# Optimization experiments

Measured on AMD Instinct MI355X. Metric: run time of the kernel, lower is better.

## Reference

```python
import jax, jax.numpy as jnp
import numpy as np

HIDDEN = 2048
EXPERTS = 8
INTER = 1024
TOP_K = 2
AUX_LOSS_WEIGHT = 0.01
TOKENS = 8192


def setup_inputs() -> dict:
    key = jax.random.key(0)
    k_x, k_g, k_w1, k_w2 = jax.random.split(key, 4)
    x = jax.random.normal(k_x, (TOKENS, HIDDEN), dtype=jnp.float32)
    # nn.Linear(hidden, experts, bias=False): weight is [E, H], applied as x @ W^T
    gate_w = jax.random.normal(k_g, (EXPERTS, HIDDEN), dtype=jnp.float32) * 0.02
    w1 = jax.random.normal(k_w1, (EXPERTS, HIDDEN, INTER), dtype=jnp.float32) * 0.02
    w2 = jax.random.normal(k_w2, (EXPERTS, INTER, HIDDEN), dtype=jnp.float32) * 0.02
    return {"x": x, "gate_w": gate_w, "w1": w1, "w2": w2}


def _moe_forward(x, gate_w, w1, w2):
    E = gate_w.shape[0]
    logits = x @ gate_w.T                              # [T, E]
    probs = jax.nn.softmax(logits, axis=-1)            # [T, E]
    topk_w, topk_idx = jax.lax.top_k(probs, TOP_K)     # [T, K]
    topk_w = topk_w / jnp.sum(topk_w, axis=-1, keepdims=True)

    # load-balancing aux loss: E * sum_e f_e * P_e
    one_hot = jax.nn.one_hot(topk_idx, E, dtype=probs.dtype)   # [T, K, E]
    f = jnp.mean(jnp.sum(one_hot, axis=1), axis=0)             # fraction of tokens per expert
    P = jnp.mean(probs, axis=0)                                # mean router prob per expert
    aux_loss = AUX_LOSS_WEIGHT * E * jnp.sum(f * P)

    # grouped expert MLP (dense-over-experts formulation, same math as
    # permute -> grouped GEMM -> unpermute):
    h = jnp.einsum('th,ehi->tei', x, w1)               # [T, E, I]
    h = jax.nn.gelu(h)
    y = jnp.einsum('tei,eih->teh', h, w2)              # [T, E, H]

    # combine: gather each token's top-k expert outputs and weight them
    y_sel = jnp.take_along_axis(y, topk_idx[:, :, None], axis=1)  # [T, K, H]
    out = jnp.sum(y_sel * topk_w[:, :, None], axis=1)             # [T, H]
    return out, aux_loss


def reference(x, gate_w, w1, w2):
    return _moe_forward(x, gate_w, w1, w2)
```

## Files before the change

### kernel.cpp

```cpp
#include <hip/hip_runtime.h>
#include <hip/hip_fp16.h>
#include <cmath>

#define T_TOKENS 8192
#define HID 2048
#define NEXP 8
#define INTERM 1024
#define GATE_NB 2048
#define MAX_TT 136
#define GEMM1_GRID (8 * 136)
#define GEMM2_GRID (8 * 272)

typedef _Float16 f16x8 __attribute__((ext_vector_type(8)));
typedef _Float16 f16x4 __attribute__((ext_vector_type(4)));
typedef float f32x4 __attribute__((ext_vector_type(4)));

static __device__ __forceinline__ float gelu_tanh(float v) {
    return 0.5f * v * (1.0f + tanhf(0.79788456080286535588f * (v + 0.044715f * v * v * v)));
}

static __device__ __forceinline__ void glds16(const void* g, void* l) {
    __builtin_amdgcn_global_load_lds((const __attribute__((address_space(1))) void*)g,
                                     (__attribute__((address_space(3))) void*)l, 16, 0, 0);
}

static __device__ __forceinline__ f16x8 lds_read32(const _Float16* base, int row, int chunk) {
    int phys = chunk ^ ((row >> 1) & 3);
    return *reinterpret_cast<const f16x8*>(
        reinterpret_cast<const char*>(base) + row * 64 + phys * 16);
}

static __device__ __forceinline__ void tconv_body(const float* __restrict__ in,
                                                  _Float16* __restrict__ out,
                                                  int R, int C, int bx, int by, int bz) {
    __shared__ float t[32][33];
    int r0 = by * 32, c0 = bx * 32;
    int tid = threadIdx.x;
    int r = tid >> 3, c4 = (tid & 7) * 4;
    const float4 v = *reinterpret_cast<const float4*>(&in[((size_t)bz * R + (r0 + r)) * C + c0 + c4]);
    t[r][c4 + 0] = v.x; t[r][c4 + 1] = v.y; t[r][c4 + 2] = v.z; t[r][c4 + 3] = v.w;
    __syncthreads();
    int oc = tid >> 3;
    int or4 = (tid & 7) * 4;
    f16x4 o;
    o[0] = (_Float16)t[or4 + 0][oc];
    o[1] = (_Float16)t[or4 + 1][oc];
    o[2] = (_Float16)t[or4 + 2][oc];
    o[3] = (_Float16)t[or4 + 3][oc];
    *reinterpret_cast<f16x4*>(&out[((size_t)bz * C + (c0 + oc)) * R + r0 + or4]) = o;
}

static __device__ __forceinline__ void gate_body(const float* __restrict__ x,
                                                 const float* __restrict__ gw,
                                                 _Float16* __restrict__ xh,
                                                 int* __restrict__ tk_idx, float* __restrict__ tk_w,
                                                 int* __restrict__ part_cnt,
                                                 double* __restrict__ part_sumP, int gid) {
    __shared__ double sds[4][NEXP];
    __shared__ int sci[4][NEXP];
    int w = threadIdx.x >> 6;
    int lane = threadIdx.x & 63;
    int t = gid * 4 + w;

    const float4* xr = (const float4*)(x + (size_t)t * HID);
    _Float16* xo = xh + (size_t)t * HID;
    double acc[NEXP];
#pragma unroll
    for (int e = 0; e < NEXP; e++) acc[e] = 0.0;
#pragma unroll
    for (int i = 0; i < HID / 256; i++) {
        float4 xv = xr[i * 64 + lane];
        f16x4 h;
        h[0] = (_Float16)xv.x; h[1] = (_Float16)xv.y;
        h[2] = (_Float16)xv.z; h[3] = (_Float16)xv.w;
        *reinterpret_cast<f16x4*>(xo + i * 256 + lane * 4) = h;
#pragma unroll
        for (int e = 0; e < NEXP; e++) {
            float4 gv = ((const float4*)(gw + (size_t)e * HID))[i * 64 + lane];
            acc[e] += (double)xv.x * (double)gv.x + (double)xv.y * (double)gv.y
                    + (double)xv.z * (double)gv.z + (double)xv.w * (double)gv.w;
        }
    }
#pragma unroll
    for (int e = 0; e < NEXP; e++) {
#pragma unroll
        for (int off = 32; off > 0; off >>= 1) acc[e] += __shfl_xor(acc[e], off, 64);
    }
    double mx = acc[0];
#pragma unroll
    for (int e = 1; e < NEXP; e++) mx = acc[e] > mx ? acc[e] : mx;
    double ex[NEXP];
    double sum = 0.0;
#pragma unroll
    for (int e = 0; e < NEXP; e++) { ex[e] = exp(acc[e] - mx); sum += ex[e]; }
    int i0 = 0;
#pragma unroll
    for (int e = 1; e < NEXP; e++) if (ex[e] > ex[i0]) i0 = e;
    int i1 = (i0 == 0) ? 1 : 0;
#pragma unroll
    for (int e = 0; e < NEXP; e++) if (e != i0 && ex[e] > ex[i1]) i1 = e;
    double p0 = ex[i0], p1 = ex[i1];
    double t2 = p0 + p1;
    if (lane == 0) {
        tk_idx[2 * t] = i0; tk_idx[2 * t + 1] = i1;
        tk_w[2 * t] = (float)(p0 / t2); tk_w[2 * t + 1] = (float)(p1 / t2);
#pragma unroll
        for (int e = 0; e < NEXP; e++) {
            sds[w][e] = ex[e] / sum;
            sci[w][e] = (e == i0 ? 1 : 0) + (e == i1 ? 1 : 0);
        }
    }
    __syncthreads();
    if (threadIdx.x < NEXP) {
        int e = threadIdx.x;
        part_sumP[e * GATE_NB + gid] = sds[0][e] + sds[1][e] + sds[2][e] + sds[3][e];
        part_cnt[e * GATE_NB + gid]  = sci[0][e] + sci[1][e] + sci[2][e] + sci[3][e];
    }
}

__global__ __launch_bounds__(256) void prep_kernel(const float* __restrict__ x,
                                                   const float* __restrict__ gw,
                                                   const float* __restrict__ w1,
                                                   const float* __restrict__ w2,
                                                   _Float16* __restrict__ xh,
                                                   _Float16* __restrict__ w1t,
                                                   _Float16* __restrict__ w2t,
                                                   int* __restrict__ tk_idx, float* __restrict__ tk_w,
                                                   int* __restrict__ part_cnt,
                                                   double* __restrict__ part_sumP) {
    int bid = blockIdx.x;
    if (bid < 16384) {
        int bx = bid & 31, by = (bid >> 5) & 63, bz = bid >> 11;
        tconv_body(w1, w1t, HID, INTERM, bx, by, bz);
    } else if (bid < 32768) {
        int r = bid - 16384;
        int bx = r & 63, by = (r >> 6) & 31, bz = r >> 11;
        tconv_body(w2, w2t, INTERM, HID, bx, by, bz);
    } else {
        gate_body(x, gw, xh, tk_idx, tk_w, part_cnt, part_sumP, bid - 32768);
    }
}

__global__ __launch_bounds__(256) void finalize_kernel(const int* __restrict__ part_cnt,
                                                       const double* __restrict__ part_sumP,
                                                       int* __restrict__ cnt, int* __restrict__ offs,
                                                       int* __restrict__ cursor,
                                                       int* __restrict__ ttab,
                                                       int* __restrict__ nmt,
                                                       float* __restrict__ aux_out) {
    __shared__ double swv[4];
    __shared__ int cwv[4];
    __shared__ double sE[NEXP];
    __shared__ int cE[NEXP];
    int w = threadIdx.x >> 6;
    int lane = threadIdx.x & 63;
    for (int e = 0; e < NEXP; e++) {
        double s = 0.0; int c = 0;
        for (int j = threadIdx.x; j < GATE_NB; j += 256) {
            s += part_sumP[e * GATE_NB + j];
            c += part_cnt[e * GATE_NB + j];
        }
#pragma unroll
        for (int off = 32; off > 0; off >>= 1) {
            s += __shfl_xor(s, off, 64);
            c += __shfl_xor(c, off, 64);
        }
        if (lane == 0) { swv[w] = s; cwv[w] = c; }
        __syncthreads();
        if (threadIdx.x == 0) {
            sE[e] = swv[0] + swv[1] + swv[2] + swv[3];
            cE[e] = cwv[0] + cwv[1] + cwv[2] + cwv[3];
        }
        __syncthreads();
    }
    if (threadIdx.x == 0) {
        int off = 0;
        double aux = 0.0;
        int idx = 0;
#pragma unroll
        for (int e = 0; e < NEXP; e++) {
            cnt[e] = cE[e];
            offs[e] = off;
            off += cE[e];
            cursor[e] = 0;
            aux += ((double)cE[e] / (double)T_TOKENS) * (sE[e] / (double)T_TOKENS);
            int mt = (cE[e] + 127) >> 7;
            for (int m = 0; m < mt; m++) ttab[idx++] = (e << 16) | m;
        }
        nmt[0] = idx;
        for (; idx < MAX_TT; idx++) ttab[idx] = -1;
        aux_out[0] = (float)(0.01 * (double)NEXP * aux);
    }
}

__global__ void scatter_kernel(const int* __restrict__ tk_idx, const float* __restrict__ tk_w,
                               const int* __restrict__ offs, int* __restrict__ cursor,
                               int* __restrict__ row_tok, float* __restrict__ row_w,
                               int* __restrict__ tok_row) {
    int t = blockIdx.x * blockDim.x + threadIdx.x;
    int lane = threadIdx.x & 63;
    unsigned long long below = (lane == 0) ? 0ull : ((~0ull) >> (64 - lane));
    for (int k = 0; k < 2; k++) {
        int e = tk_idx[2 * t + k];
        float wv = tk_w[2 * t + k];
        int pos = 0;
#pragma unroll
        for (int ee = 0; ee < NEXP; ee++) {
            unsigned long long m = __ballot(e == ee);
            if (e == ee) {
                int rank = (int)__popcll(m & below);
                int leader = (int)__ffsll((unsigned long long)m) - 1;
                int b = 0;
                if (lane == leader) b = atomicAdd(&cursor[ee], (int)__popcll(m));
                b = __shfl(b, leader, 64);
                pos = b + rank;
            }
        }
        int r = offs[e] + pos;
        row_tok[r] = t;
        row_w[r] = wv;
        tok_row[2 * t + k] = r;
    }
}

template<bool GATHER, bool GELU, int KTOT, int NX>
__global__ __launch_bounds__(256, 4) void gemmf_kernel(
    const _Float16* __restrict__ Aglob,
    const _Float16* __restrict__ Bglob,
    const int* __restrict__ cnt, const int* __restrict__ offs,
    const int* __restrict__ row_tok,
    const int* __restrict__ ttab,
    const int* __restrict__ nmt,
    _Float16* __restrict__ Out, int Ncols)
{
    constexpr int NT = KTOT / 32;
    __shared__ __align__(16) _Float16 As[2][128][32];
    __shared__ __align__(16) _Float16 Bs[2][128][32];

    int n_items = nmt[0] * NX;
    int chunk = (n_items + 7) >> 3;
    int xcd = blockIdx.x & 7;
    int i = blockIdx.x >> 3;
    if (i >= chunk) return;
    int it = xcd * chunk + i;
    if (it >= n_items) return;

    int tid = threadIdx.x;
    int w = tid >> 6, lane = tid & 63;
    int wr = w >> 1, wc = w & 1;
    int fr = lane & 15, fq = lane >> 4;

    int srow = lane >> 2;
    int lc = (lane & 3) ^ ((lane >> 3) & 3);

    _Float16* ldsA = &As[0][0][0] + w * 1024;
    _Float16* ldsB = &Bs[0][0][0] + w * 1024;

    int ent = ttab[it / NX];
    int e = ent >> 16;
    int m0 = (ent & 0xffff) << 7;
    int Ne = cnt[e];
    int base = offs[e];
    int n0 = (it & (NX - 1)) << 7;

    const _Float16* aS[2];
#pragma unroll
    for (int g = 0; g < 2; g++) {
        int ar = m0 + w * 32 + g * 16 + srow; if (ar >= Ne) ar = Ne - 1;
        int id = GATHER ? row_tok[base + ar] : (base + ar);
        aS[g] = Aglob + (size_t)id * KTOT + lc * 8;
    }
    const size_t bexp = (size_t)e * Ncols * KTOT;
    const _Float16* bS[2];
#pragma unroll
    for (int g = 0; g < 2; g++)
        bS[g] = Bglob + bexp + (size_t)(n0 + w * 32 + g * 16 + srow) * KTOT + lc * 8;

#define STAGE1(S, KOFF) do {                                        \
        glds16(aS[0] + (KOFF), ldsA + (S) * 4096 + 0 * 512);        \
        glds16(aS[1] + (KOFF), ldsA + (S) * 4096 + 1 * 512);        \
        glds16(bS[0] + (KOFF), ldsB + (S) * 4096 + 0 * 512);        \
        glds16(bS[1] + (KOFF), ldsB + (S) * 4096 + 1 * 512);        \
    } while (0)

    f32x4 acc[4][4] = {};
    STAGE1(0, 0);

    for (int j = 0; j < NT; ++j) {
        int slot = j & 1;
        const _Float16* Ab = &As[slot][0][0];
        const _Float16* Bb = &Bs[slot][0][0];
        if (j + 1 < NT) {
            STAGE1(slot ^ 1, (j + 1) * 32);
            asm volatile("s_waitcnt vmcnt(4)" ::: "memory");
        } else {
            asm volatile("s_waitcnt vmcnt(0)" ::: "memory");
        }
        __builtin_amdgcn_s_barrier();

        f16x8 a_[4], b_[4];
#pragma unroll
        for (int ii = 0; ii < 4; ii++)
            a_[ii] = lds_read32(Ab, wr * 64 + ii * 16 + fr, fq);
#pragma unroll
        for (int jj = 0; jj < 4; jj++)
            b_[jj] = lds_read32(Bb, wc * 64 + jj * 16 + fr, fq);
#pragma unroll
        for (int ii = 0; ii < 4; ii++)
#pragma unroll
            for (int jj = 0; jj < 4; jj++)
                acc[ii][jj] = __builtin_amdgcn_mfma_f32_16x16x32_f16(
                    a_[ii], b_[jj], acc[ii][jj], 0, 0, 0);
        asm volatile("s_waitcnt lgkmcnt(0)" ::: "memory");
        __builtin_amdgcn_s_barrier();
    }
#undef STAGE1

#pragma unroll
    for (int mi = 0; mi < 4; mi++) {
#pragma unroll
        for (int r = 0; r < 4; r++) {
            int row = m0 + wr * 64 + mi * 16 + fq * 4 + r;
            if (row < Ne) {
                _Float16* dst = Out + (size_t)(base + row) * Ncols + n0 + wc * 64 + fr;
#pragma unroll
                for (int ni = 0; ni < 4; ni++) {
                    float v = acc[mi][ni][r];
                    if (GELU) v = gelu_tanh(v);
                    dst[ni * 16] = (_Float16)v;
                }
            }
        }
    }
}

__global__ __launch_bounds__(256) void combine_kernel(const _Float16* __restrict__ y,
                                                      const int* __restrict__ tok_row,
                                                      const float* __restrict__ tk_w,
                                                      float* __restrict__ out) {
    int t = blockIdx.x;
    int c = threadIdx.x;
    int r0 = tok_row[2 * t], r1 = tok_row[2 * t + 1];
    float w0 = tk_w[2 * t], w1 = tk_w[2 * t + 1];
    f16x8 a = reinterpret_cast<const f16x8*>(y + (size_t)r0 * HID)[c];
    f16x8 b = reinterpret_cast<const f16x8*>(y + (size_t)r1 * HID)[c];
    float4 o0, o1;
    o0.x = w0 * (float)a[0] + w1 * (float)b[0];
    o0.y = w0 * (float)a[1] + w1 * (float)b[1];
    o0.z = w0 * (float)a[2] + w1 * (float)b[2];
    o0.w = w0 * (float)a[3] + w1 * (float)b[3];
    o1.x = w0 * (float)a[4] + w1 * (float)b[4];
    o1.y = w0 * (float)a[5] + w1 * (float)b[5];
    o1.z = w0 * (float)a[6] + w1 * (float)b[6];
    o1.w = w0 * (float)a[7] + w1 * (float)b[7];
    float4* dst = reinterpret_cast<float4*>(out + (size_t)t * HID + c * 8);
    dst[0] = o0;
    dst[1] = o1;
}

extern "C" void kernel_launch(void* const* d_in, const int* in_sizes, int n_in,
                              void* d_out, int out_size, void* d_ws, size_t ws_size,
                              hipStream_t stream) {
    const float* x  = (const float*)d_in[0];
    const float* gw = (const float*)d_in[1];
    const float* w1 = (const float*)d_in[2];
    const float* w2 = (const float*)d_in[3];
    float* out = (float*)d_out;
    char* ws = (char*)d_ws;

    int*    cnt       = (int*)(ws + 0);
    int*    cursor    = (int*)(ws + 64);
    int*    offs      = (int*)(ws + 128);
    int*    nmt       = (int*)(ws + 256);
    int*    ttab      = (int*)(ws + 512);
    int*    part_cnt  = (int*)(ws + 4096);
    double* part_sumP = (double*)(ws + 131072);
    int*    row_tok   = (int*)(ws + 262144);
    float*  row_w     = (float*)(ws + 327680);
    int*    tk_idx    = (int*)(ws + 393216);
    float*  tk_w      = (float*)(ws + 458752);
    int*    tok_row   = (int*)(ws + 524288);
    const size_t OFF = 589824;
    _Float16* xh  = (_Float16*)(ws + OFF);
    _Float16* w1t = (_Float16*)(ws + OFF + (1ull << 25));
    _Float16* w2t = (_Float16*)(ws + OFF + (2ull << 25));
    _Float16* hh  = (_Float16*)(ws + OFF + (3ull << 25));
    _Float16* y   = (_Float16*)(ws + OFF);

    prep_kernel<<<32768 + GATE_NB, 256, 0, stream>>>(x, gw, w1, w2, xh, w1t, w2t,
                                                     tk_idx, tk_w, part_cnt, part_sumP);
    finalize_kernel<<<1, 256, 0, stream>>>(part_cnt, part_sumP, cnt, offs, cursor,
                                           ttab, nmt, out + (size_t)T_TOKENS * HID);
    scatter_kernel<<<T_TOKENS / 256, 256, 0, stream>>>(tk_idx, tk_w, offs, cursor,
                                                       row_tok, row_w, tok_row);

    gemmf_kernel<true, true, HID, INTERM / 128>
        <<<GEMM1_GRID, 256, 0, stream>>>(xh, w1t, cnt, offs, row_tok, ttab, nmt, hh, INTERM);
    gemmf_kernel<false, false, INTERM, HID / 128>
        <<<GEMM2_GRID, 256, 0, stream>>>(hh, w2t, cnt, offs, row_tok, ttab, nmt, y, HID);

    combine_kernel<<<T_TOKENS, 256, 0, stream>>>(y, tok_row, tk_w, out);
}
```

Before: 378.2 us.

## Overlap w2 transpose with first expert GEMM and use single-buffered GEMM2

After: 372.9 us. No clear change (-1.4%).

```diff
diff --git a/kernel.cpp b/kernel.cpp
--- a/kernel.cpp
+++ b/kernel.cpp
@@ -9,6 +9,7 @@
 #define GATE_NB 2048
 #define MAX_TT 136
 #define GEMM1_GRID (8 * 136)
+#define W2_BLOCKS 16384
 #define GEMM2_GRID (8 * 272)
 
 typedef _Float16 f16x8 __attribute__((ext_vector_type(8)));
@@ -32,21 +33,22 @@
 
 static __device__ __forceinline__ void tconv_body(const float* __restrict__ in,
                                                   _Float16* __restrict__ out,
-                                                  int R, int C, int bx, int by, int bz) {
-    __shared__ float t[32][33];
+                                                  int R, int C, int bx, int by, int bz,
+                                                  float* __restrict__ t ) {
     int r0 = by * 32, c0 = bx * 32;
     int tid = threadIdx.x;
     int r = tid >> 3, c4 = (tid & 7) * 4;
     const float4 v = *reinterpret_cast<const float4*>(&in[((size_t)bz * R + (r0 + r)) * C + c0 + c4]);
-    t[r][c4 + 0] = v.x; t[r][c4 + 1] = v.y; t[r][c4 + 2] = v.z; t[r][c4 + 3] = v.w;
+    t[r * 33 + c4 + 0] = v.x; t[r * 33 + c4 + 1] = v.y;
+    t[r * 33 + c4 + 2] = v.z; t[r * 33 + c4 + 3] = v.w;
     __syncthreads();
     int oc = tid >> 3;
     int or4 = (tid & 7) * 4;
     f16x4 o;
-    o[0] = (_Float16)t[or4 + 0][oc];
-    o[1] = (_Float16)t[or4 + 1][oc];
-    o[2] = (_Float16)t[or4 + 2][oc];
-    o[3] = (_Float16)t[or4 + 3][oc];
+    o[0] = (_Float16)t[(or4 + 0) * 33 + oc];
+    o[1] = (_Float16)t[(or4 + 1) * 33 + oc];
+    o[2] = (_Float16)t[(or4 + 2) * 33 + oc];
+    o[3] = (_Float16)t[(or4 + 3) * 33 + oc];
     *reinterpret_cast<f16x4*>(&out[((size_t)bz * C + (c0 + oc)) * R + r0 + or4]) = o;
 }
 
@@ -121,23 +123,18 @@
 __global__ __launch_bounds__(256) void prep_kernel(const float* __restrict__ x,
                                                    const float* __restrict__ gw,
                                                    const float* __restrict__ w1,
-                                                   const float* __restrict__ w2,
                                                    _Float16* __restrict__ xh,
                                                    _Float16* __restrict__ w1t,
-                                                   _Float16* __restrict__ w2t,
                                                    int* __restrict__ tk_idx, float* __restrict__ tk_w,
                                                    int* __restrict__ part_cnt,
                                                    double* __restrict__ part_sumP) {
+    __shared__ float tsh[32 * 33];
     int bid = blockIdx.x;
     if (bid < 16384) {
         int bx = bid & 31, by = (bid >> 5) & 63, bz = bid >> 11;
-        tconv_body(w1, w1t, HID, INTERM, bx, by, bz);
-    } else if (bid < 32768) {
-        int r = bid - 16384;
-        int bx = r & 63, by = (r >> 6) & 31, bz = r >> 11;
-        tconv_body(w2, w2t, INTERM, HID, bx, by, bz);
+        tconv_body(w1, w1t, HID, INTERM, bx, by, bz, tsh);
     } else {
-        gate_body(x, gw, xh, tk_idx, tk_w, part_cnt, part_sumP, bid - 32768);
+        gate_body(x, gw, xh, tk_idx, tk_w, part_cnt, part_sumP, bid - 16384);
     }
 }
 
@@ -223,7 +220,7 @@
     }
 }
 
-template<bool GATHER, bool GELU, int KTOT, int NX>
+template<bool GATHER, bool GELU, int KTOT, int NX, bool FUSE>
 __global__ __launch_bounds__(256, 4) void gemmf_kernel(
     const _Float16* __restrict__ Aglob,
     const _Float16* __restrict__ Bglob,
@@ -231,11 +228,20 @@
     const int* __restrict__ row_tok,
     const int* __restrict__ ttab,
     const int* __restrict__ nmt,
-    _Float16* __restrict__ Out, int Ncols)
+    _Float16* __restrict__ Out, int Ncols,
+    const float* __restrict__ w2in, _Float16* __restrict__ w2out)
 {
     constexpr int NT = KTOT / 32;
     __shared__ __align__(16) _Float16 As[2][128][32];
     __shared__ __align__(16) _Float16 Bs[2][128][32];
+
+    if (FUSE && blockIdx.x >= GEMM1_GRID) {
+        int b = blockIdx.x - GEMM1_GRID;
+        int bx = b & 63, by = (b >> 6) & 31, bz = b >> 11;
+        tconv_body(w2in, w2out, INTERM, HID, bx, by, bz,
+                   reinterpret_cast<float*>(&As[0][0][0]));
+        return;
+    }
 
     int n_items = nmt[0] * NX;
     int chunk = (n_items + 7) >> 3;
@@ -329,6 +335,98 @@
                     if (GELU) v = gelu_tanh(v);
                     dst[ni * 16] = (_Float16)v;
                 }
+            }
+        }
+    }
+}
+
+template<int KTOT, int NX>
+__global__ __launch_bounds__(256, 4) void gemms_kernel(
+    const _Float16* __restrict__ Aglob,
+    const _Float16* __restrict__ Bglob,
+    const int* __restrict__ cnt, const int* __restrict__ offs,
+    const int* __restrict__ ttab,
+    const int* __restrict__ nmt,
+    _Float16* __restrict__ Out, int Ncols)
+{
+    constexpr int NT = KTOT / 32;
+    __shared__ __align__(16) _Float16 As[128][32];
+    __shared__ __align__(16) _Float16 Bs[128][32];
+
+    int n_items = nmt[0] * NX;
+    int chunk = (n_items + 7) >> 3;
+    int xcd = blockIdx.x & 7;
+    int i = blockIdx.x >> 3;
+    if (i >= chunk) return;
+    int it = xcd * chunk + i;
+    if (it >= n_items) return;
+
+    int tid = threadIdx.x;
+    int w = tid >> 6, lane = tid & 63;
+    int wr = w >> 1, wc = w & 1;
+    int fr = lane & 15, fq = lane >> 4;
+
+    int srow = lane >> 2;
+    int lc = (lane & 3) ^ ((lane >> 3) & 3);
+
+    _Float16* ldsA = &As[0][0] + w * 1024;
+    _Float16* ldsB = &Bs[0][0] + w * 1024;
+
+    int ent = ttab[it / NX];
+    int e = ent >> 16;
+    int m0 = (ent & 0xffff) << 7;
+    int Ne = cnt[e];
+    int base = offs[e];
+    int n0 = (it & (NX - 1)) << 7;
+
+    const _Float16* aS[2];
+#pragma unroll
+    for (int g = 0; g < 2; g++) {
+        int ar = m0 + w * 32 + g * 16 + srow; if (ar >= Ne) ar = Ne - 1;
+        aS[g] = Aglob + (size_t)(base + ar) * KTOT + lc * 8;
+    }
+    const size_t bexp = (size_t)e * Ncols * KTOT;
+    const _Float16* bS[2];
+#pragma unroll
+    for (int g = 0; g < 2; g++)
+        bS[g] = Bglob + bexp + (size_t)(n0 + w * 32 + g * 16 + srow) * KTOT + lc * 8;
+
+    f32x4 acc[4][4] = {};
+
+    for (int j = 0; j < NT; ++j) {
+        int koff = j * 32;
+        glds16(aS[0] + koff, ldsA + 0 * 512);
+        glds16(aS[1] + koff, ldsA + 1 * 512);
+        glds16(bS[0] + koff, ldsB + 0 * 512);
+        glds16(bS[1] + koff, ldsB + 1 * 512);
+        __syncthreads();
+
+        f16x8 a_[4], b_[4];
+#pragma unroll
+        for (int ii = 0; ii < 4; ii++)
+            a_[ii] = lds_read32(&As[0][0], wr * 64 + ii * 16 + fr, fq);
+#pragma unroll
+        for (int jj = 0; jj < 4; jj++)
+            b_[jj] = lds_read32(&Bs[0][0], wc * 64 + jj * 16 + fr, fq);
+#pragma unroll
+        for (int ii = 0; ii < 4; ii++)
+#pragma unroll
+            for (int jj = 0; jj < 4; jj++)
+                acc[ii][jj] = __builtin_amdgcn_mfma_f32_16x16x32_f16(
+                    a_[ii], b_[jj], acc[ii][jj], 0, 0, 0);
+        __syncthreads();
+    }
+
+#pragma unroll
+    for (int mi = 0; mi < 4; mi++) {
+#pragma unroll
+        for (int r = 0; r < 4; r++) {
+            int row = m0 + wr * 64 + mi * 16 + fq * 4 + r;
+            if (row < Ne) {
+                _Float16* dst = Out + (size_t)(base + row) * Ncols + n0 + wc * 64 + fr;
+#pragma unroll
+                for (int ni = 0; ni < 4; ni++)
+                    dst[ni * 16] = (_Float16)acc[mi][ni][r];
             }
         }
     }
@@ -387,17 +485,18 @@
     _Float16* hh  = (_Float16*)(ws + OFF + (3ull << 25));
     _Float16* y   = (_Float16*)(ws + OFF);
 
-    prep_kernel<<<32768 + GATE_NB, 256, 0, stream>>>(x, gw, w1, w2, xh, w1t, w2t,
+    prep_kernel<<<16384 + GATE_NB, 256, 0, stream>>>(x, gw, w1, xh, w1t,
                                                      tk_idx, tk_w, part_cnt, part_sumP);
     finalize_kernel<<<1, 256, 0, stream>>>(part_cnt, part_sumP, cnt, offs, cursor,
                                            ttab, nmt, out + (size_t)T_TOKENS * HID);
     scatter_kernel<<<T_TOKENS / 256, 256, 0, stream>>>(tk_idx, tk_w, offs, cursor,
                                                        row_tok, row_w, tok_row);
 
-    gemmf_kernel<true, true, HID, INTERM / 128>
-        <<<GEMM1_GRID, 256, 0, stream>>>(xh, w1t, cnt, offs, row_tok, ttab, nmt, hh, INTERM);
-    gemmf_kernel<false, false, INTERM, HID / 128>
-        <<<GEMM2_GRID, 256, 0, stream>>>(hh, w2t, cnt, offs, row_tok, ttab, nmt, y, HID);
+    gemmf_kernel<true, true, HID, INTERM / 128, true>
+        <<<GEMM1_GRID + W2_BLOCKS, 256, 0, stream>>>(xh, w1t, cnt, offs, row_tok, ttab, nmt,
+                                                     hh, INTERM, w2, w2t);
+    gemms_kernel<INTERM, HID / 128>
+        <<<GEMM2_GRID, 256, 0, stream>>>(hh, w2t, cnt, offs, ttab, nmt, y, HID);
 
     combine_kernel<<<T_TOKENS, 256, 0, stream>>>(y, tok_row, tk_w, out);
 }
```

## Overlap w2 transpose with first expert GEMM and use single-buffered BK=64 tiles

Applied to the files above, without the earlier changes.

Result: faster. 333.7 us (-11.8%).

```diff
diff --git a/kernel.cpp b/kernel.cpp
--- a/kernel.cpp
+++ b/kernel.cpp
@@ -9,6 +9,7 @@
 #define GATE_NB 2048
 #define MAX_TT 136
 #define GEMM1_GRID (8 * 136)
+#define W2_BLOCKS 16384
 #define GEMM2_GRID (8 * 272)
 
 typedef _Float16 f16x8 __attribute__((ext_vector_type(8)));
@@ -24,29 +25,30 @@
                                      (__attribute__((address_space(3))) void*)l, 16, 0, 0);
 }
 
-static __device__ __forceinline__ f16x8 lds_read32(const _Float16* base, int row, int chunk) {
-    int phys = chunk ^ ((row >> 1) & 3);
+static __device__ __forceinline__ f16x8 lds_read(const _Float16* base, int row, int chunk) {
+    int phys = chunk ^ (row & 7);
     return *reinterpret_cast<const f16x8*>(
-        reinterpret_cast<const char*>(base) + row * 64 + phys * 16);
+        reinterpret_cast<const char*>(base) + row * 128 + phys * 16);
 }
 
 static __device__ __forceinline__ void tconv_body(const float* __restrict__ in,
                                                   _Float16* __restrict__ out,
-                                                  int R, int C, int bx, int by, int bz) {
-    __shared__ float t[32][33];
+                                                  int R, int C, int bx, int by, int bz,
+                                                  float* __restrict__ t ) {
     int r0 = by * 32, c0 = bx * 32;
     int tid = threadIdx.x;
     int r = tid >> 3, c4 = (tid & 7) * 4;
     const float4 v = *reinterpret_cast<const float4*>(&in[((size_t)bz * R + (r0 + r)) * C + c0 + c4]);
-    t[r][c4 + 0] = v.x; t[r][c4 + 1] = v.y; t[r][c4 + 2] = v.z; t[r][c4 + 3] = v.w;
+    t[r * 33 + c4 + 0] = v.x; t[r * 33 + c4 + 1] = v.y;
+    t[r * 33 + c4 + 2] = v.z; t[r * 33 + c4 + 3] = v.w;
     __syncthreads();
     int oc = tid >> 3;
     int or4 = (tid & 7) * 4;
     f16x4 o;
-    o[0] = (_Float16)t[or4 + 0][oc];
-    o[1] = (_Float16)t[or4 + 1][oc];
-    o[2] = (_Float16)t[or4 + 2][oc];
-    o[3] = (_Float16)t[or4 + 3][oc];
+    o[0] = (_Float16)t[(or4 + 0) * 33 + oc];
+    o[1] = (_Float16)t[(or4 + 1) * 33 + oc];
+    o[2] = (_Float16)t[(or4 + 2) * 33 + oc];
+    o[3] = (_Float16)t[(or4 + 3) * 33 + oc];
     *reinterpret_cast<f16x4*>(&out[((size_t)bz * C + (c0 + oc)) * R + r0 + or4]) = o;
 }
 
@@ -121,23 +123,18 @@
 __global__ __launch_bounds__(256) void prep_kernel(const float* __restrict__ x,
                                                    const float* __restrict__ gw,
                                                    const float* __restrict__ w1,
-                                                   const float* __restrict__ w2,
                                                    _Float16* __restrict__ xh,
                                                    _Float16* __restrict__ w1t,
-                                                   _Float16* __restrict__ w2t,
                                                    int* __restrict__ tk_idx, float* __restrict__ tk_w,
                                                    int* __restrict__ part_cnt,
                                                    double* __restrict__ part_sumP) {
+    __shared__ float tsh[32 * 33];
     int bid = blockIdx.x;
     if (bid < 16384) {
         int bx = bid & 31, by = (bid >> 5) & 63, bz = bid >> 11;
-        tconv_body(w1, w1t, HID, INTERM, bx, by, bz);
-    } else if (bid < 32768) {
-        int r = bid - 16384;
-        int bx = r & 63, by = (r >> 6) & 31, bz = r >> 11;
-        tconv_body(w2, w2t, INTERM, HID, bx, by, bz);
+        tconv_body(w1, w1t, HID, INTERM, bx, by, bz, tsh);
     } else {
-        gate_body(x, gw, xh, tk_idx, tk_w, part_cnt, part_sumP, bid - 32768);
+        gate_body(x, gw, xh, tk_idx, tk_w, part_cnt, part_sumP, bid - 16384);
     }
 }
 
@@ -223,19 +220,28 @@
     }
 }
 
-template<bool GATHER, bool GELU, int KTOT, int NX>
-__global__ __launch_bounds__(256, 4) void gemmf_kernel(
+template<bool GATHER, bool GELU, int KTOT, int NX, bool FUSE>
+__global__ __launch_bounds__(256, 4) void gemmk_kernel(
     const _Float16* __restrict__ Aglob,
     const _Float16* __restrict__ Bglob,
     const int* __restrict__ cnt, const int* __restrict__ offs,
     const int* __restrict__ row_tok,
     const int* __restrict__ ttab,
     const int* __restrict__ nmt,
-    _Float16* __restrict__ Out, int Ncols)
+    _Float16* __restrict__ Out, int Ncols,
+    const float* __restrict__ w2in, _Float16* __restrict__ w2out)
 {
-    constexpr int NT = KTOT / 32;
-    __shared__ __align__(16) _Float16 As[2][128][32];
-    __shared__ __align__(16) _Float16 Bs[2][128][32];
+    constexpr int NT = KTOT / 64;
+    __shared__ __align__(16) _Float16 As[128][64];
+    __shared__ __align__(16) _Float16 Bs[128][64];
+
+    if (FUSE && blockIdx.x >= GEMM1_GRID) {
+        int b = blockIdx.x - GEMM1_GRID;
+        int bx = b & 63, by = (b >> 6) & 31, bz = b >> 11;
+        tconv_body(w2in, w2out, INTERM, HID, bx, by, bz,
+                   reinterpret_cast<float*>(&As[0][0]));
+        return;
+    }
 
     int n_items = nmt[0] * NX;
     int chunk = (n_items + 7) >> 3;
@@ -250,11 +256,11 @@
     int wr = w >> 1, wc = w & 1;
     int fr = lane & 15, fq = lane >> 4;
 
-    int srow = lane >> 2;
-    int lc = (lane & 3) ^ ((lane >> 3) & 3);
-
-    _Float16* ldsA = &As[0][0][0] + w * 1024;
-    _Float16* ldsB = &Bs[0][0][0] + w * 1024;
+    int srow = lane >> 3;
+    int lc = (lane & 7) ^ srow;
+
+    _Float16* ldsA = &As[w * 32][0];
+    _Float16* ldsB = &Bs[w * 32][0];
 
     int ent = ttab[it / NX];
     int e = ent >> 16;
@@ -263,58 +269,47 @@
     int base = offs[e];
     int n0 = (it & (NX - 1)) << 7;
 
-    const _Float16* aS[2];
-#pragma unroll
-    for (int g = 0; g < 2; g++) {
-        int ar = m0 + w * 32 + g * 16 + srow; if (ar >= Ne) ar = Ne - 1;
+    const _Float16* aS[4];
+#pragma unroll
+    for (int g = 0; g < 4; g++) {
+        int ar = m0 + w * 32 + g * 8 + srow; if (ar >= Ne) ar = Ne - 1;
         int id = GATHER ? row_tok[base + ar] : (base + ar);
         aS[g] = Aglob + (size_t)id * KTOT + lc * 8;
     }
     const size_t bexp = (size_t)e * Ncols * KTOT;
-    const _Float16* bS[2];
-#pragma unroll
-    for (int g = 0; g < 2; g++)
-        bS[g] = Bglob + bexp + (size_t)(n0 + w * 32 + g * 16 + srow) * KTOT + lc * 8;
-
-#define STAGE1(S, KOFF) do {                                        \
-        glds16(aS[0] + (KOFF), ldsA + (S) * 4096 + 0 * 512);        \
-        glds16(aS[1] + (KOFF), ldsA + (S) * 4096 + 1 * 512);        \
-        glds16(bS[0] + (KOFF), ldsB + (S) * 4096 + 0 * 512);        \
-        glds16(bS[1] + (KOFF), ldsB + (S) * 4096 + 1 * 512);        \
-    } while (0)
+    const _Float16* bS[4];
+#pragma unroll
+    for (int g = 0; g < 4; g++)
+        bS[g] = Bglob + bexp + (size_t)(n0 + w * 32 + g * 8 + srow) * KTOT + lc * 8;
 
     f32x4 acc[4][4] = {};
-    STAGE1(0, 0);
 
     for (int j = 0; j < NT; ++j) {
-        int slot = j & 1;
-        const _Float16* Ab = &As[slot][0][0];
-        const _Float16* Bb = &Bs[slot][0][0];
-        if (j + 1 < NT) {
-            STAGE1(slot ^ 1, (j + 1) * 32);
-            asm volatile("s_waitcnt vmcnt(4)" ::: "memory");
-        } else {
-            asm volatile("s_waitcnt vmcnt(0)" ::: "memory");
-        }
-        __builtin_amdgcn_s_barrier();
-
-        f16x8 a_[4], b_[4];
-#pragma unroll
-        for (int ii = 0; ii < 4; ii++)
-            a_[ii] = lds_read32(Ab, wr * 64 + ii * 16 + fr, fq);
-#pragma unroll
-        for (int jj = 0; jj < 4; jj++)
-            b_[jj] = lds_read32(Bb, wc * 64 + jj * 16 + fr, fq);
-#pragma unroll
-        for (int ii = 0; ii < 4; ii++)
+        int koff = j * 64;
+#pragma unroll
+        for (int g = 0; g < 4; g++) glds16(aS[g] + koff, ldsA + g * 512);
+#pragma unroll
+        for (int g = 0; g < 4; g++) glds16(bS[g] + koff, ldsB + g * 512);
+        __syncthreads();
+
+#pragma unroll
+        for (int ks = 0; ks < 2; ks++) {
+            f16x8 a_[4], b_[4];
+#pragma unroll
+            for (int ii = 0; ii < 4; ii++)
+                a_[ii] = lds_read(&As[0][0], wr * 64 + ii * 16 + fr, ks * 4 + fq);
 #pragma unroll
             for (int jj = 0; jj < 4; jj++)
-                acc[ii][jj] = __builtin_amdgcn_mfma_f32_16x16x32_f16(
-                    a_[ii], b_[jj], acc[ii][jj], 0, 0, 0);
-        asm volatile("s_waitcnt lgkmcnt(0)" ::: "memory");
-        __builtin_amdgcn_s_barrier();
-    }
-#undef STAGE1
+                b_[jj] = lds_read(&Bs[0][0], wc * 64 + jj * 16 + fr, ks * 4 + fq);
+#pragma unroll
+            for (int ii = 0; ii < 4; ii++)
+#pragma unroll
+                for (int jj = 0; jj < 4; jj++)
+                    acc[ii][jj] = __builtin_amdgcn_mfma_f32_16x16x32_f16(
+                        a_[ii], b_[jj], acc[ii][jj], 0, 0, 0);
+        }
+        __syncthreads();
+    }
 
 #pragma unroll
     for (int mi = 0; mi < 4; mi++) {
@@ -387,17 +382,19 @@
     _Float16* hh  = (_Float16*)(ws + OFF + (3ull << 25));
     _Float16* y   = (_Float16*)(ws + OFF);
 
-    prep_kernel<<<32768 + GATE_NB, 256, 0, stream>>>(x, gw, w1, w2, xh, w1t, w2t,
+    prep_kernel<<<16384 + GATE_NB, 256, 0, stream>>>(x, gw, w1, xh, w1t,
                                                      tk_idx, tk_w, part_cnt, part_sumP);
     finalize_kernel<<<1, 256, 0, stream>>>(part_cnt, part_sumP, cnt, offs, cursor,
                                            ttab, nmt, out + (size_t)T_TOKENS * HID);
     scatter_kernel<<<T_TOKENS / 256, 256, 0, stream>>>(tk_idx, tk_w, offs, cursor,
                                                        row_tok, row_w, tok_row);
 
-    gemmf_kernel<true, true, HID, INTERM / 128>
-        <<<GEMM1_GRID, 256, 0, stream>>>(xh, w1t, cnt, offs, row_tok, ttab, nmt, hh, INTERM);
-    gemmf_kernel<false, false, INTERM, HID / 128>
-        <<<GEMM2_GRID, 256, 0, stream>>>(hh, w2t, cnt, offs, row_tok, ttab, nmt, y, HID);
+    gemmk_kernel<true, true, HID, INTERM / 128, true>
+        <<<GEMM1_GRID + W2_BLOCKS, 256, 0, stream>>>(xh, w1t, cnt, offs, row_tok, ttab, nmt,
+                                                     hh, INTERM, w2, w2t);
+    gemmk_kernel<false, false, INTERM, HID / 128, false>
+        <<<GEMM2_GRID, 256, 0, stream>>>(hh, w2t, cnt, offs, row_tok, ttab, nmt,
+                                         y, HID, nullptr, nullptr);
 
     combine_kernel<<<T_TOKENS, 256, 0, stream>>>(y, tok_row, tk_w, out);
 }
```
